# Kernel optimization log

Measured on AMD Instinct MI355X. Metric: run time of the kernel, lower is better.

## Reference

```python
import jax, jax.numpy as jnp
import numpy as np

B, N, D = 8, 1024, 768
NHEAD = 4
N_EDGES = 3
ITERS = 2
DK = D // NHEAD


def setup_inputs() -> dict:
    key = jax.random.key(0)
    ks = jax.random.split(key, 12)
    s = 0.02
    return {
        "nodes_embed": jax.random.normal(ks[0], (B, N, D), dtype=jnp.float32),
        "node_adj": jax.random.randint(ks[1], (B, N, N), 0, 4, dtype=jnp.int32),
        # per-edge-type Q/K linear layers (torch Linear: y = x W^T + b; stored here as [in,out])
        "Wq": jax.random.normal(ks[2], (N_EDGES, D, D), dtype=jnp.float32) * s,
        "bq": jax.random.normal(ks[3], (N_EDGES, D), dtype=jnp.float32) * s,
        "Wk": jax.random.normal(ks[4], (N_EDGES, D, D), dtype=jnp.float32) * s,
        "bk": jax.random.normal(ks[5], (N_EDGES, D), dtype=jnp.float32) * s,
        # GCN weights: shared across heads (self.blocks reuses the same Sequential), distinct per iter
        "gcn_W": jax.random.normal(ks[6], (ITERS, D, D), dtype=jnp.float32) * s,
        "gcn_b": jnp.zeros((ITERS, D), dtype=jnp.float32),
        # aggregate_W: Linear(D*nhead -> D), stored as [D*nhead, D]
        "W_agg": jax.random.normal(ks[7], (D * NHEAD, D), dtype=jnp.float32) * s,
        "b_agg": jnp.zeros((D,), dtype=jnp.float32),
    }


def reference(nodes_embed, node_adj, Wq, bq, Wk, bk, gcn_W, gcn_b, W_agg, b_agg):
    Bv, Nv, Dv = nodes_embed.shape
    h, dk = NHEAD, DK
    adj = node_adj[:, None, :, :]  # [B,1,N,N]
    scale = 1.0 / jnp.sqrt(jnp.asarray(dk, nodes_embed.dtype))

    scores = jnp.zeros((Bv, h, Nv, Nv), dtype=nodes_embed.dtype)
    for e in range(N_EDGES):  # small fixed edge-type loop
        q = (nodes_embed @ Wq[e] + bq[e]).reshape(Bv, Nv, h, dk).transpose(0, 2, 1, 3)  # [B,h,N,dk]
        k = (nodes_embed @ Wk[e] + bk[e]).reshape(Bv, Nv, h, dk).transpose(0, 2, 1, 3)
        s = jnp.einsum('bhnd,bhmd->bhnm', q, k) * scale
        scores = scores + jnp.where(adj == e + 1, s, jnp.zeros((), s.dtype))
    scores = jnp.where(scores == 0, jnp.asarray(-1e9, scores.dtype), scores)
    attn = jax.nn.softmax(scores, axis=-1)          # [B,h,N,N]
    ga = jnp.transpose(attn, (1, 0, 2, 3))          # [h,B,N,N]

    # GCN blocks, vectorized over heads; weights shared across heads
    X = jnp.broadcast_to(nodes_embed, (h, Bv, Nv, Dv))  # [h,B,N,D]
    for i in range(ITERS):
        H = jnp.einsum('hbnd,de->hbne', X, gcn_W[i])
        sum_nei = jnp.einsum('hbnm,hbmd->hbnd', ga, H)
        degs = jnp.sum(ga, axis=-1, keepdims=True)       # [h,B,N,1]
        dst = sum_nei / degs + gcn_b[i]
        X = X + jax.nn.relu(dst)

    # torch.cat over heads along feature dim -> [B,N,h*D]
    cat = jnp.transpose(X, (1, 2, 0, 3)).reshape(Bv, Nv, h * Dv)
    out = cat @ W_agg + b_agg
    return out, ga
```

## Files before the change

### kernel.cpp

```cpp
#include <hip/hip_runtime.h>

typedef long long i64;
typedef unsigned short u16;
typedef __attribute__((ext_vector_type(8))) short short8;
typedef __attribute__((ext_vector_type(4))) float f32x4;

#define Bv 8
#define Nv 1024
#define Dv 768
#define Hh 4
#define DKv 192
#define BND ((i64)Bv * Nv * Dv)
#define HBND ((i64)Hh * BND)

__device__ __forceinline__ u16 f2bf(float f) {
    unsigned u = __builtin_bit_cast(unsigned, f);
    u += 0x7fffu + ((u >> 16) & 1u);
    return (u16)(u >> 16);
}
__device__ __forceinline__ float bf2f(u16 h) {
    unsigned u = ((unsigned)h) << 16;
    return __builtin_bit_cast(float, u);
}

__device__ __forceinline__ void gl_lds16(const u16* g, u16* l) {
    __builtin_amdgcn_global_load_lds(
        (const __attribute__((address_space(1))) void*)g,
        (__attribute__((address_space(3))) void*)l, 16, 0, 0);
}

template <int EPI, bool CATK, int ORD, int NBN, int NBM, int NZ>
__global__ __launch_bounds__(256) void gemm_bf16(
    const u16* __restrict__ A, i64 sA, int lda,
    const u16* __restrict__ Bt, i64 sBt, int ldbt, int zmaskBt,
    const float* __restrict__ bias, i64 sBias, const float* __restrict__ bias2,
    void* __restrict__ Cv, i64 sC, int ldc, int K, int koff)
{
    __shared__ u16 Asb[128 * 64];
    __shared__ u16 Bsb[128 * 64];

    const int L = (blockIdx.x & 7) * ((NBN * NBM * NZ) >> 3) + (blockIdx.x >> 3);
    int bn, bm, z;
    if (ORD == 0) {
        bn = L % NBN; const int t2 = L / NBN; bm = t2 % NBM; z = t2 / NBM;
    } else {
        bn = L % NBN; const int t2 = L / NBN; z = t2 % NZ; bm = t2 / NZ;
    }

    A  += (i64)z * sA;
    Bt += (i64)(z & zmaskBt) * sBt;
    const float* bp = bias;
    int zb = z;
    if (bias2 != nullptr && z >= NZ / 2) { bp = bias2; zb = z - NZ / 2; }
    if (bp) bp += (i64)zb * sBias;
    const int kb = z * koff;

    const int bmp = bm * 128, bnp = bn * 128;
    const int tid = threadIdx.x;
    const int w = tid >> 6, l = tid & 63;
    const int wr = w >> 1, wc = w & 1;
    const int kgrp = l >> 4, lr = l & 15;

    const u16* Ab = A + (i64)bmp * lda;
    const u16* Bb = Bt + (i64)bnp * ldbt;

    f32x4 acc[4][4];
    #pragma unroll
    for (int i = 0; i < 4; ++i)
        #pragma unroll
        for (int j = 0; j < 4; ++j)
            acc[i][j] = (f32x4){0.f, 0.f, 0.f, 0.f};

    for (int k0i = 0; k0i < K; k0i += 64) {
        const int k0 = kb + k0i;
        if (k0i) __syncthreads();
        #pragma unroll
        for (int t = 0; t < 4; ++t) {
            const int idx = t * 256 + tid;
            const int r = idx >> 3, s = idx & 7;
            const int ss = s ^ (r & 7);
            const u16* src;
            if (CATK) {
                src = A + (i64)(k0 / Dv) * BND + (i64)(bmp + r) * Dv + (k0 % Dv) + ss * 8;
            } else {
                src = Ab + (i64)r * lda + k0 + ss * 8;
            }
            gl_lds16(src, &Asb[(t * 256 + w * 64) * 8]);
        }
        #pragma unroll
        for (int t = 0; t < 4; ++t) {
            const int idx = t * 256 + tid;
            const int r = idx >> 3, s = idx & 7;
            const int ss = s ^ (r & 7);
            gl_lds16(Bb + (i64)r * ldbt + k0 + ss * 8, &Bsb[(t * 256 + w * 64) * 8]);
        }
        __syncthreads();

        #pragma unroll
        for (int ks = 0; ks < 2; ++ks) {
            const int slot = ks * 4 + kgrp;
            short8 a[4], b[4];
            #pragma unroll
            for (int i = 0; i < 4; ++i) {
                const int r = wc * 64 + i * 16 + lr;
                a[i] = *(const short8*)&Bsb[r * 64 + ((slot ^ (r & 7)) << 3)];
            }
            #pragma unroll
            for (int j = 0; j < 4; ++j) {
                const int r = wr * 64 + j * 16 + lr;
                b[j] = *(const short8*)&Asb[r * 64 + ((slot ^ (r & 7)) << 3)];
            }
            #pragma unroll
            for (int i = 0; i < 4; ++i)
                #pragma unroll
                for (int j = 0; j < 4; ++j)
                    acc[i][j] = __builtin_amdgcn_mfma_f32_16x16x32_bf16(
                        a[i], b[j], acc[i][j], 0, 0, 0);
        }
    }

    f32x4 bj[4];
    #pragma unroll
    for (int i = 0; i < 4; ++i) {
        const int nb = bnp + wc * 64 + i * 16 + kgrp * 4;
        bj[i] = bp ? *(const f32x4*)&bp[nb] : (f32x4){0.f, 0.f, 0.f, 0.f};
    }

    #pragma unroll
    for (int j = 0; j < 4; ++j) {
        const int m = bmp + wr * 64 + j * 16 + lr;
        #pragma unroll
        for (int i = 0; i < 4; ++i) {
            const int nb = bnp + wc * 64 + i * 16 + kgrp * 4;
            const i64 off = (i64)z * sC + (i64)m * ldc + nb;
            f32x4 v = acc[i][j] + bj[i];
            if (EPI == 0) {
                *(f32x4*)&((float*)Cv)[off] = v;
            } else if (EPI == 1) {
                ushort4 o;
                o.x = f2bf(v[0]); o.y = f2bf(v[1]);
                o.z = f2bf(v[2]); o.w = f2bf(v[3]);
                *(ushort4*)&((u16*)Cv)[off] = o;
            } else {
                u16* xp = (u16*)Cv + off;
                ushort4 old = *(const ushort4*)xp;
                ushort4 o;
                o.x = f2bf(bf2f(old.x) + fmaxf(v[0], 0.f));
                o.y = f2bf(bf2f(old.y) + fmaxf(v[1], 0.f));
                o.z = f2bf(bf2f(old.z) + fmaxf(v[2], 0.f));
                o.w = f2bf(bf2f(old.w) + fmaxf(v[3], 0.f));
                *(ushort4*)xp = o;
            }
        }
    }
}

__global__ __launch_bounds__(256) void scores_mfma(
    const u16* __restrict__ qb, const u16* __restrict__ kb,
    const int* __restrict__ adj, u16* __restrict__ sb)
{
    __shared__ u16 Qs[2][64 * 64];
    __shared__ u16 Ks[2][64 * 64];

    const int bid = blockIdx.x;
    const int b = bid & 7;
    const int t2 = bid >> 3;
    const int h = t2 & 3;
    const int mt = (t2 >> 2) & 15;
    const int nt = t2 >> 6;
    const int m0 = mt * 64, n0 = nt * 64;
    const int zga = h * 8 + b;

    const int tid = threadIdx.x;
    const int w = tid >> 6, l = tid & 63;
    const int wr = w >> 1, wc = w & 1;
    const int kgrp = l >> 4, lr = l & 15;

    const i64 qoff = ((i64)b * Nv + n0) * Dv + h * DKv;
    const i64 koff = ((i64)b * Nv + m0) * Dv + h * DKv;

#define STAGE_SC(ci_, buf_) { \
    const int e_ = (ci_) / 3, k0_ = ((ci_) % 3) * 64; \
    const u16* qe_ = qb + (i64)e_ * BND + qoff; \
    const u16* ke_ = kb + (i64)e_ * BND + koff; \
    _Pragma("unroll") \
    for (int t = 0; t < 2; ++t) { \
        const int idx2 = t * 256 + tid; \
        const int r = idx2 >> 3, s = idx2 & 7; \
        const int ss = s ^ (r & 7); \
        gl_lds16(qe_ + (i64)r * Dv + k0_ + ss * 8, &Qs[buf_][(t * 256 + w * 64) * 8]); \
        gl_lds16(ke_ + (i64)r * Dv + k0_ + ss * 8, &Ks[buf_][(t * 256 + w * 64) * 8]); \
    } }

    int4 adjv[2][2];
    #pragma unroll
    for (int i = 0; i < 2; ++i) {
        const int mb = m0 + wc * 32 + i * 16 + kgrp * 4;
        #pragma unroll
        for (int j = 0; j < 2; ++j) {
            const int n = n0 + wr * 32 + j * 16 + lr;
            adjv[i][j] = *(const int4*)&adj[((i64)b * Nv + n) * Nv + mb];
        }
    }

    f32x4 acc[3][2][2];
    #pragma unroll
    for (int e = 0; e < 3; ++e)
        #pragma unroll
        for (int i = 0; i < 2; ++i)
            #pragma unroll
            for (int j = 0; j < 2; ++j)
                acc[e][i][j] = (f32x4){0.f, 0.f, 0.f, 0.f};

    STAGE_SC(0, 0)

    #pragma unroll
    for (int ci = 0; ci < 9; ++ci) {
        const int cur = ci & 1;
        if (ci < 8) {
            if (cur) { STAGE_SC(ci + 1, 0) } else { STAGE_SC(ci + 1, 1) }
            asm volatile("s_waitcnt vmcnt(4)" ::: "memory");
        } else {
            asm volatile("s_waitcnt vmcnt(0)" ::: "memory");
        }
        __builtin_amdgcn_s_barrier();
        asm volatile("" ::: "memory");

        const int e = ci / 3;
        #pragma unroll
        for (int ks = 0; ks < 2; ++ks) {
            const int slot = ks * 4 + kgrp;
            short8 a[2], bq2[2];
            #pragma unroll
            for (int i = 0; i < 2; ++i) {
                const int r = wc * 32 + i * 16 + lr;
                a[i] = *(const short8*)&Ks[cur][r * 64 + ((slot ^ (r & 7)) << 3)];
            }
            #pragma unroll
            for (int j = 0; j < 2; ++j) {
                const int r = wr * 32 + j * 16 + lr;
                bq2[j] = *(const short8*)&Qs[cur][r * 64 + ((slot ^ (r & 7)) << 3)];
            }
            #pragma unroll
            for (int i = 0; i < 2; ++i)
                #pragma unroll
                for (int j = 0; j < 2; ++j)
                    acc[e][i][j] = __builtin_amdgcn_mfma_f32_16x16x32_bf16(
                        a[i], bq2[j], acc[e][i][j], 0, 0, 0);
        }

        asm volatile("s_waitcnt lgkmcnt(0)" ::: "memory");
        __builtin_amdgcn_s_barrier();
    }
#undef STAGE_SC

    const float scale = 0.07216878364870323f;
    #pragma unroll
    for (int i = 0; i < 2; ++i) {
        const int mb = m0 + wc * 32 + i * 16 + kgrp * 4;
        #pragma unroll
        for (int j = 0; j < 2; ++j) {
            const int n = n0 + wr * 32 + j * 16 + lr;
            const int av[4] = {adjv[i][j].x, adjv[i][j].y, adjv[i][j].z, adjv[i][j].w};
            ushort4 o;
            #pragma unroll
            for (int rg = 0; rg < 4; ++rg) {
                float f = 0.f;
                if (av[rg] == 1) f = acc[0][i][j][rg];
                else if (av[rg] == 2) f = acc[1][i][j][rg];
                else if (av[rg] == 3) f = acc[2][i][j][rg];
                f *= scale;
                if (f == 0.f) f = -1e9f;
                ((u16*)&o)[rg] = f2bf(f);
            }
            *(ushort4*)&sb[((i64)zga * Nv + n) * Nv + mb] = o;
        }
    }
}

__global__ __launch_bounds__(256) void softmax_k(const u16* __restrict__ sb,
                                                 float* __restrict__ ga,
                                                 u16* __restrict__ gab)
{
    const i64 row = blockIdx.x;
    const int tid = threadIdx.x;
    const int wid = tid >> 6, lane = tid & 63;

    ushort4 sv = *(const ushort4*)&sb[row * (i64)Nv + tid * 4];
    float4 v;
    v.x = bf2f(sv.x); v.y = bf2f(sv.y); v.z = bf2f(sv.z); v.w = bf2f(sv.w);

    float m = fmaxf(fmaxf(v.x, v.y), fmaxf(v.z, v.w));
    #pragma unroll
    for (int o = 32; o >= 1; o >>= 1) m = fmaxf(m, __shfl_xor(m, o));

    __shared__ float red[4];
    if (lane == 0) red[wid] = m;
    __syncthreads();
    m = fmaxf(fmaxf(red[0], red[1]), fmaxf(red[2], red[3]));

    float e0 = expf(v.x - m), e1 = expf(v.y - m), e2 = expf(v.z - m), e3 = expf(v.w - m);
    float s = e0 + e1 + e2 + e3;
    #pragma unroll
    for (int o = 32; o >= 1; o >>= 1) s += __shfl_xor(s, o);
    __syncthreads();
    if (lane == 0) red[wid] = s;
    __syncthreads();
    s = red[0] + red[1] + red[2] + red[3];

    const float inv = 1.0f / s;
    float4 o;
    o.x = e0 * inv; o.y = e1 * inv; o.z = e2 * inv; o.w = e3 * inv;
    *(float4*)&ga[row * (i64)Nv + tid * 4] = o;

    ushort4 ob;
    ob.x = f2bf(o.x); ob.y = f2bf(o.y); ob.z = f2bf(o.z); ob.w = f2bf(o.w);
    *(ushort4*)&gab[row * (i64)Nv + tid * 4] = ob;
}

__global__ __launch_bounds__(256) void prep_k(const float* __restrict__ nodes,
                                              u16* __restrict__ nodesb,
                                              u16* __restrict__ Xb)
{
    const i64 i = (i64)blockIdx.x * 256 + threadIdx.x;
    float4 v = ((const float4*)nodes)[i];
    ushort4 o;
    o.x = f2bf(v.x); o.y = f2bf(v.y); o.z = f2bf(v.z); o.w = f2bf(v.w);
    ((ushort4*)nodesb)[i] = o;
    const i64 q4 = BND / 4;
    #pragma unroll
    for (int h = 0; h < Hh; ++h) ((ushort4*)Xb)[(i64)h * q4 + i] = o;
}

__global__ __launch_bounds__(256) void trans_all(
    const float* __restrict__ Wq, const float* __restrict__ Wk,
    const float* __restrict__ gcnW, const float* __restrict__ Wagg,
    u16* __restrict__ wqkt, u16* __restrict__ gcnWt, u16* __restrict__ waggt)
{
    const int z = blockIdx.z;
    const i64 W768 = (i64)768 * 768;
    const float* src;
    u16* dst;
    int ldo;
    if (z < 3)      { src = Wq + z * W768;        dst = wqkt + z * W768;          ldo = 768; }
    else if (z < 6) { src = Wk + (z - 3) * W768;  dst = wqkt + (i64)z * W768;     ldo = 768; }
    else if (z < 8) { src = gcnW + (z - 6) * W768; dst = gcnWt + (i64)(z - 6) * W768; ldo = 768; }
    else            { src = Wagg + (i64)(z - 8) * W768; dst = waggt + (i64)(z - 8) * 768; ldo = 3072; }

    __shared__ u16 t[32][33];
    const int c0 = blockIdx.x * 32, r0 = blockIdx.y * 32;
    const int tx = threadIdx.x & 31, ty = threadIdx.x >> 5;
    #pragma unroll
    for (int i = ty; i < 32; i += 8)
        t[i][tx] = f2bf(src[(i64)(r0 + i) * 768 + c0 + tx]);
    __syncthreads();
    #pragma unroll
    for (int i = ty; i < 32; i += 8)
        dst[(i64)(c0 + i) * ldo + r0 + tx] = t[tx][i];
}

__global__ __launch_bounds__(256) void addbias_k(
    const float* __restrict__ p0, const float* __restrict__ p1,
    const float* __restrict__ bias, float* __restrict__ out)
{
    const i64 i4 = (i64)blockIdx.x * 256 + threadIdx.x;
    const int nb = (int)((i4 * 4) % Dv);
    float4 a = ((const float4*)p0)[i4];
    float4 b = ((const float4*)p1)[i4];
    float4 bv = *(const float4*)&bias[nb];
    float4 o;
    o.x = a.x + b.x + bv.x; o.y = a.y + b.y + bv.y;
    o.z = a.z + b.z + bv.z; o.w = a.w + b.w + bv.w;
    ((float4*)out)[i4] = o;
}

extern "C" void kernel_launch(void* const* d_in, const int* in_sizes, int n_in,
                              void* d_out, int out_size, void* d_ws, size_t ws_size,
                              hipStream_t stream)
{
    const float* nodes = (const float*)d_in[0];
    const int*   adj   = (const int*)d_in[1];
    const float* Wq    = (const float*)d_in[2];
    const float* bq    = (const float*)d_in[3];
    const float* Wk    = (const float*)d_in[4];
    const float* bk    = (const float*)d_in[5];
    const float* gcnW  = (const float*)d_in[6];
    const float* gcnb  = (const float*)d_in[7];
    const float* Wagg  = (const float*)d_in[8];
    const float* bagg  = (const float*)d_in[9];

    float* out = (float*)d_out;
    float* gaf = out + BND;

    const i64 W768 = (i64)768 * 768;
    const i64 HTZ  = (i64)768 * 1024;
    u16* ws     = (u16*)d_ws;
    u16* qb     = ws;
    u16* kb2    = ws + 3 * BND;
    u16* gab    = ws;
    u16* nodesb = ws + 6 * BND;
    u16* gcnWt  = nodesb + BND;
    u16* waggt  = gcnWt + 2 * W768;
    u16* Xb     = waggt + 4 * W768;
    u16* Htz    = Xb + HBND;
    u16* wqkt   = Htz;
    u16* sbuf   = Htz;
    float* part = (float*)Htz;

    dim3 blk(256);

    prep_k<<<dim3((unsigned)(BND / 4 / 256)), blk, 0, stream>>>(nodes, nodesb, Xb);
    trans_all<<<dim3(24, 24, 12), blk, 0, stream>>>(Wq, Wk, gcnW, Wagg, wqkt, gcnWt, waggt);

    gemm_bf16<1, false, 1, 6, 64, 6><<<dim3(2304), blk, 0, stream>>>(
        nodesb, 0, Dv, wqkt, W768, Dv, -1, bq, Dv, bk, qb, BND, Dv, Dv, 0);

    scores_mfma<<<dim3(8192), blk, 0, stream>>>(qb, kb2, adj, sbuf);

    softmax_k<<<dim3(Hh * Bv * Nv), blk, 0, stream>>>(sbuf, gaf, gab);

    for (int it = 0; it < 2; ++it) {
        if (it == 0) {
            gemm_bf16<1, false, 0, 8, 6, 8><<<dim3(384), blk, 0, stream>>>(
                gcnWt, 0, Dv, nodesb, (i64)Nv * Dv, Dv, 7, nullptr, 0, nullptr,
                Htz, HTZ, 1024, Dv, 0);
            gemm_bf16<2, false, 0, 6, 8, 32><<<dim3(1536), blk, 0, stream>>>(
                gab, (i64)Nv * Nv, Nv, Htz, HTZ, 1024, 7, gcnb, 0, nullptr,
                Xb, (i64)Nv * Dv, Dv, Nv, 0);
        } else {
            gemm_bf16<1, false, 0, 8, 6, 32><<<dim3(1536), blk, 0, stream>>>(
                gcnWt + W768, 0, Dv, Xb, (i64)Nv * Dv, Dv, 31, nullptr, 0, nullptr,
                Htz, HTZ, 1024, Dv, 0);
            gemm_bf16<2, false, 0, 6, 8, 32><<<dim3(1536), blk, 0, stream>>>(
                gab, (i64)Nv * Nv, Nv, Htz, HTZ, 1024, 31, gcnb + (i64)Dv, 0, nullptr,
                Xb, (i64)Nv * Dv, Dv, Nv, 0);
        }
    }

    gemm_bf16<0, true, 0, 6, 64, 2><<<dim3(768), blk, 0, stream>>>(
        Xb, 0, Dv, waggt, 0, Hh * Dv, -1, nullptr, 0, nullptr,
        part, BND, Dv, (Hh * Dv) / 2, (Hh * Dv) / 2);

    addbias_k<<<dim3((unsigned)(BND / 4 / 256)), blk, 0, stream>>>(
        part, part + BND, bagg, out);
}
```

Measured before the change: 542.7 us.

## Enlarge scores kernel tiles to 128x128 and fold edge selection per type

The scores kernel now computes 128x128 output tiles per block instead of 64x64, with each wave holding a 4x4 grid of MFMA accumulators. This quadruples reuse of each staged Q/K tile and cuts the block count from 8192 to 2048. Edge types are processed one after another with a single accumulator set, and the adjacency mask is applied into a final register tile after each type, which keeps register use bounded. In exchange, the double-buffered async staging pipeline is replaced by single-buffered loads fenced by syncthreads, so load latency is no longer overlapped with compute. Adjacency is also re-read from global memory once per edge type.

After: 572.3 us. 1.05x slower.

```diff
diff --git a/kernel.cpp b/kernel.cpp
--- a/kernel.cpp
+++ b/kernel.cpp
@@ -159,16 +159,16 @@
     const u16* __restrict__ qb, const u16* __restrict__ kb,
     const int* __restrict__ adj, u16* __restrict__ sb)
 {
-    __shared__ u16 Qs[2][64 * 64];
-    __shared__ u16 Ks[2][64 * 64];
+    __shared__ u16 Qs[128 * 64];
+    __shared__ u16 Ks[128 * 64];
 
     const int bid = blockIdx.x;
     const int b = bid & 7;
     const int t2 = bid >> 3;
     const int h = t2 & 3;
-    const int mt = (t2 >> 2) & 15;
-    const int nt = t2 >> 6;
-    const int m0 = mt * 64, n0 = nt * 64;
+    const int tile = t2 >> 2;
+    const int mt = tile & 7, nt = tile >> 3;
+    const int m0 = mt * 128, n0 = nt * 128;
     const int zga = h * 8 + b;
 
     const int tid = threadIdx.x;
@@ -176,100 +176,95 @@
     const int wr = w >> 1, wc = w & 1;
     const int kgrp = l >> 4, lr = l & 15;
 
-    const i64 qoff = ((i64)b * Nv + n0) * Dv + h * DKv;
-    const i64 koff = ((i64)b * Nv + m0) * Dv + h * DKv;
-
-#define STAGE_SC(ci_, buf_) { \
-    const int e_ = (ci_) / 3, k0_ = ((ci_) % 3) * 64; \
-    const u16* qe_ = qb + (i64)e_ * BND + qoff; \
-    const u16* ke_ = kb + (i64)e_ * BND + koff; \
-    _Pragma("unroll") \
-    for (int t = 0; t < 2; ++t) { \
-        const int idx2 = t * 256 + tid; \
-        const int r = idx2 >> 3, s = idx2 & 7; \
-        const int ss = s ^ (r & 7); \
-        gl_lds16(qe_ + (i64)r * Dv + k0_ + ss * 8, &Qs[buf_][(t * 256 + w * 64) * 8]); \
-        gl_lds16(ke_ + (i64)r * Dv + k0_ + ss * 8, &Ks[buf_][(t * 256 + w * 64) * 8]); \
-    } }
-
-    int4 adjv[2][2];
-    #pragma unroll
-    for (int i = 0; i < 2; ++i) {
-        const int mb = m0 + wc * 32 + i * 16 + kgrp * 4;
-        #pragma unroll
-        for (int j = 0; j < 2; ++j) {
-            const int n = n0 + wr * 32 + j * 16 + lr;
-            adjv[i][j] = *(const int4*)&adj[((i64)b * Nv + n) * Nv + mb];
-        }
-    }
-
-    f32x4 acc[3][2][2];
-    #pragma unroll
-    for (int e = 0; e < 3; ++e)
-        #pragma unroll
-        for (int i = 0; i < 2; ++i)
-            #pragma unroll
-            for (int j = 0; j < 2; ++j)
-                acc[e][i][j] = (f32x4){0.f, 0.f, 0.f, 0.f};
-
-    STAGE_SC(0, 0)
-
-    #pragma unroll
-    for (int ci = 0; ci < 9; ++ci) {
-        const int cur = ci & 1;
-        if (ci < 8) {
-            if (cur) { STAGE_SC(ci + 1, 0) } else { STAGE_SC(ci + 1, 1) }
-            asm volatile("s_waitcnt vmcnt(4)" ::: "memory");
-        } else {
-            asm volatile("s_waitcnt vmcnt(0)" ::: "memory");
-        }
-        __builtin_amdgcn_s_barrier();
-        asm volatile("" ::: "memory");
-
-        const int e = ci / 3;
-        #pragma unroll
-        for (int ks = 0; ks < 2; ++ks) {
-            const int slot = ks * 4 + kgrp;
-            short8 a[2], bq2[2];
-            #pragma unroll
-            for (int i = 0; i < 2; ++i) {
-                const int r = wc * 32 + i * 16 + lr;
-                a[i] = *(const short8*)&Ks[cur][r * 64 + ((slot ^ (r & 7)) << 3)];
-            }
-            #pragma unroll
-            for (int j = 0; j < 2; ++j) {
-                const int r = wr * 32 + j * 16 + lr;
-                bq2[j] = *(const short8*)&Qs[cur][r * 64 + ((slot ^ (r & 7)) << 3)];
-            }
-            #pragma unroll
-            for (int i = 0; i < 2; ++i)
+    const u16* qbase = qb + ((i64)b * Nv + n0) * Dv + h * DKv;
+    const u16* kbase = kb + ((i64)b * Nv + m0) * Dv + h * DKv;
+
+    const float scale = 0.07216878364870323f;
+
+    f32x4 fin[4][4];
+    #pragma unroll
+    for (int i = 0; i < 4; ++i)
+        #pragma unroll
+        for (int j = 0; j < 4; ++j)
+            fin[i][j] = (f32x4){0.f, 0.f, 0.f, 0.f};
+
+    for (int e = 0; e < 3; ++e) {
+        const u16* qe = qbase + (i64)e * BND;
+        const u16* ke = kbase + (i64)e * BND;
+
+        f32x4 acc[4][4];
+        #pragma unroll
+        for (int i = 0; i < 4; ++i)
+            #pragma unroll
+            for (int j = 0; j < 4; ++j)
+                acc[i][j] = (f32x4){0.f, 0.f, 0.f, 0.f};
+
+        for (int k0 = 0; k0 < DKv; k0 += 64) {
+            __syncthreads();
+            #pragma unroll
+            for (int t = 0; t < 4; ++t) {
+                const int idx = t * 256 + tid;
+                const int r = idx >> 3, s = idx & 7;
+                const int ss = s ^ (r & 7);
+                gl_lds16(qe + (i64)r * Dv + k0 + ss * 8, &Qs[(t * 256 + w * 64) * 8]);
+            }
+            #pragma unroll
+            for (int t = 0; t < 4; ++t) {
+                const int idx = t * 256 + tid;
+                const int r = idx >> 3, s = idx & 7;
+                const int ss = s ^ (r & 7);
+                gl_lds16(ke + (i64)r * Dv + k0 + ss * 8, &Ks[(t * 256 + w * 64) * 8]);
+            }
+            __syncthreads();
+
+            #pragma unroll
+            for (int ks = 0; ks < 2; ++ks) {
+                const int slot = ks * 4 + kgrp;
+                short8 a[4], bq2[4];
                 #pragma unroll
-                for (int j = 0; j < 2; ++j)
-                    acc[e][i][j] = __builtin_amdgcn_mfma_f32_16x16x32_bf16(
-                        a[i], bq2[j], acc[e][i][j], 0, 0, 0);
-        }
-
-        asm volatile("s_waitcnt lgkmcnt(0)" ::: "memory");
-        __builtin_amdgcn_s_barrier();
-    }
-#undef STAGE_SC
-
-    const float scale = 0.07216878364870323f;
-    #pragma unroll
-    for (int i = 0; i < 2; ++i) {
-        const int mb = m0 + wc * 32 + i * 16 + kgrp * 4;
-        #pragma unroll
-        for (int j = 0; j < 2; ++j) {
-            const int n = n0 + wr * 32 + j * 16 + lr;
-            const int av[4] = {adjv[i][j].x, adjv[i][j].y, adjv[i][j].z, adjv[i][j].w};
+                for (int i = 0; i < 4; ++i) {
+                    const int r = wc * 64 + i * 16 + lr;
+                    a[i] = *(const short8*)&Ks[r * 64 + ((slot ^ (r & 7)) << 3)];
+                }
+                #pragma unroll
+                for (int j = 0; j < 4; ++j) {
+                    const int r = wr * 64 + j * 16 + lr;
+                    bq2[j] = *(const short8*)&Qs[r * 64 + ((slot ^ (r & 7)) << 3)];
+                }
+                #pragma unroll
+                for (int i = 0; i < 4; ++i)
+                    #pragma unroll
+                    for (int j = 0; j < 4; ++j)
+                        acc[i][j] = __builtin_amdgcn_mfma_f32_16x16x32_bf16(
+                            a[i], bq2[j], acc[i][j], 0, 0, 0);
+            }
+        }
+
+        #pragma unroll
+        for (int i = 0; i < 4; ++i) {
+            const int mb = m0 + wc * 64 + i * 16 + kgrp * 4;
+            #pragma unroll
+            for (int j = 0; j < 4; ++j) {
+                const int n = n0 + wr * 64 + j * 16 + lr;
+                const int4 av = *(const int4*)&adj[((i64)b * Nv + n) * Nv + mb];
+                if (av.x == e + 1) fin[i][j][0] = acc[i][j][0] * scale;
+                if (av.y == e + 1) fin[i][j][1] = acc[i][j][1] * scale;
+                if (av.z == e + 1) fin[i][j][2] = acc[i][j][2] * scale;
+                if (av.w == e + 1) fin[i][j][3] = acc[i][j][3] * scale;
+            }
+        }
+    }
+
+    #pragma unroll
+    for (int i = 0; i < 4; ++i) {
+        const int mb = m0 + wc * 64 + i * 16 + kgrp * 4;
+        #pragma unroll
+        for (int j = 0; j < 4; ++j) {
+            const int n = n0 + wr * 64 + j * 16 + lr;
             ushort4 o;
             #pragma unroll
             for (int rg = 0; rg < 4; ++rg) {
-                float f = 0.f;
-                if (av[rg] == 1) f = acc[0][i][j][rg];
-                else if (av[rg] == 2) f = acc[1][i][j][rg];
-                else if (av[rg] == 3) f = acc[2][i][j][rg];
-                f *= scale;
+                float f = fin[i][j][rg];
                 if (f == 0.f) f = -1e9f;
                 ((u16*)&o)[rg] = f2bf(f);
             }
@@ -415,7 +410,7 @@
     gemm_bf16<1, false, 1, 6, 64, 6><<<dim3(2304), blk, 0, stream>>>(
         nodesb, 0, Dv, wqkt, W768, Dv, -1, bq, Dv, bk, qb, BND, Dv, Dv, 0);
 
-    scores_mfma<<<dim3(8192), blk, 0, stream>>>(qb, kb2, adj, sbuf);
+    scores_mfma<<<dim3(2048), blk, 0, stream>>>(qb, kb2, adj, sbuf);
 
     softmax_k<<<dim3(Hh * Bv * Nv), blk, 0, stream>>>(sbuf, gaf, gab);
 
```

## Add 256x256-tile 8-wave GEMM with phased prefetch for GCN aggregation update

Applied to the files above, without the earlier changes.

Replaces the 128x128-tile GEMM used for the attention-times-H aggregation and X residual update with a new 512-thread kernel. Each block computes a 256x256 output tile, double-buffers LDS, and splits each K-step into four phases that interleave global-to-LDS prefetch of the next tile with MFMA work, raising wave priority during the MFMA bursts. The larger tile cuts global and LDS traffic per FLOP and launches 384 blocks instead of 1536. In exchange it uses much more LDS and registers per block, and the smaller grid may leave some compute units with uneven load.

Result: slower. 566.7 us (+4.4%).

```diff
diff --git a/kernel.cpp b/kernel.cpp
--- a/kernel.cpp
+++ b/kernel.cpp
@@ -28,6 +28,8 @@
         (const __attribute__((address_space(1))) void*)g,
         (__attribute__((address_space(3))) void*)l, 16, 0, 0);
 }
+
+#define VMCNT(n) asm volatile("s_waitcnt vmcnt(" #n ")" ::: "memory")
 
 template <int EPI, bool CATK, int ORD, int NBN, int NBM, int NZ>
 __global__ __launch_bounds__(256) void gemm_bf16(
@@ -155,6 +157,143 @@
     }
 }
 
+__global__ __launch_bounds__(512, 2) void gemm256_xupd(
+    const u16* __restrict__ A, i64 sA, int lda,
+    const u16* __restrict__ Bt, i64 sBt, int ldbt, int zmask,
+    const float* __restrict__ bias,
+    u16* __restrict__ X, i64 sX, int ldx, int K)
+{
+    __shared__ u16 Asb[2][256 * 64];
+    __shared__ u16 Bsb[2][256 * 64];
+
+    const int L = (blockIdx.x & 7) * 48 + (blockIdx.x >> 3);
+    const int bn = L % 3;
+    const int t2 = L / 3;
+    const int bm = t2 & 3;
+    const int z  = t2 >> 2;
+
+    const u16* Ab = A + (i64)z * sA + (i64)(bm * 256) * lda;
+    const u16* Bb = Bt + (i64)(z & zmask) * sBt + (i64)(bn * 256) * ldbt;
+
+    const int tid = threadIdx.x;
+    const int w = tid >> 6, l = tid & 63;
+    const int wr = w >> 2;
+    const int wc = w & 3;
+    const int kgrp = l >> 4, lr = l & 15;
+    const int srow = tid >> 3;
+    const int scol = tid & 7;
+
+    f32x4 acc[8][4];
+    #pragma unroll
+    for (int f = 0; f < 8; ++f)
+        #pragma unroll
+        for (int g = 0; g < 4; ++g)
+            acc[f][g] = (f32x4){0.f, 0.f, 0.f, 0.f};
+
+    short8 bfr[4][2];
+
+#define STG_B(bb_, k0_, q_) { \
+    const int r_ = (q_) * 64 + srow; \
+    const int ss_ = scol ^ (r_ & 7); \
+    gl_lds16(Bb + (i64)r_ * ldbt + (k0_) + ss_ * 8, &Bsb[bb_][(r_ * 8 + scol) * 8]); }
+#define STG_A(bb_, k0_, p_) { \
+    const int r_ = (srow < 32) ? ((p_) * 32 + srow) : (128 + (p_) * 32 + (srow - 32)); \
+    const int ss_ = scol ^ (r_ & 7); \
+    gl_lds16(Ab + (i64)r_ * lda + (k0_) + ss_ * 8, &Asb[bb_][(r_ * 8 + scol) * 8]); }
+#define STG_PH(P_, bb_, k0_) \
+    if ((P_) == 0) { STG_B(bb_, k0_, 0) STG_B(bb_, k0_, 1) } \
+    else if ((P_) == 1) { STG_B(bb_, k0_, 2) STG_B(bb_, k0_, 3) } \
+    else if ((P_) == 2) { STG_A(bb_, k0_, 0) STG_A(bb_, k0_, 1) } \
+    else { STG_A(bb_, k0_, 2) STG_A(bb_, k0_, 3) }
+
+#define PHASE(P_, VMN_, cur_, DOPF_, nxt_, k0n_) { \
+    VMCNT(VMN_); \
+    __builtin_amdgcn_s_barrier(); \
+    asm volatile("" ::: "memory"); \
+    if ((P_) == 0) { \
+        _Pragma("unroll") \
+        for (int g = 0; g < 4; ++g) \
+            _Pragma("unroll") \
+            for (int ks = 0; ks < 2; ++ks) { \
+                const int r_ = wc * 64 + g * 16 + lr; \
+                const int sl_ = ks * 4 + kgrp; \
+                bfr[g][ks] = *(const short8*)&Bsb[cur_][r_ * 64 + ((sl_ ^ (r_ & 7)) << 3)]; \
+            } \
+    } \
+    short8 afr[2][2]; \
+    _Pragma("unroll") \
+    for (int i = 0; i < 2; ++i) \
+        _Pragma("unroll") \
+        for (int ks = 0; ks < 2; ++ks) { \
+            const int r_ = wr * 128 + (2 * (P_) + i) * 16 + lr; \
+            const int sl_ = ks * 4 + kgrp; \
+            afr[i][ks] = *(const short8*)&Asb[cur_][r_ * 64 + ((sl_ ^ (r_ & 7)) << 3)]; \
+        } \
+    if (DOPF_) { STG_PH(P_, nxt_, k0n_) } \
+    __builtin_amdgcn_s_setprio(1); \
+    _Pragma("unroll") \
+    for (int i = 0; i < 2; ++i) \
+        _Pragma("unroll") \
+        for (int g = 0; g < 4; ++g) \
+            _Pragma("unroll") \
+            for (int ks = 0; ks < 2; ++ks) \
+                acc[2 * (P_) + i][g] = __builtin_amdgcn_mfma_f32_16x16x32_bf16( \
+                    bfr[g][ks], afr[i][ks], acc[2 * (P_) + i][g], 0, 0, 0); \
+    __builtin_amdgcn_s_setprio(0); }
+
+    const int NT = K / 64;
+
+    STG_PH(0, 0, 0) STG_PH(1, 0, 0) STG_PH(2, 0, 0) STG_PH(3, 0, 0)
+    VMCNT(0);
+    __builtin_amdgcn_s_barrier();
+    asm volatile("" ::: "memory");
+
+    for (int kt = 0; kt < NT - 1; ++kt) {
+        const int cur = kt & 1, nxt = cur ^ 1;
+        const int k0n = (kt + 1) * 64;
+        PHASE(0, 3, cur, 1, nxt, k0n)
+        PHASE(1, 4, cur, 1, nxt, k0n)
+        PHASE(2, 5, cur, 1, nxt, k0n)
+        PHASE(3, 6, cur, 1, nxt, k0n)
+    }
+    {
+        const int cur = (NT - 1) & 1;
+        PHASE(0, 3, cur, 0, 0, 0)
+        PHASE(1, 2, cur, 0, 0, 0)
+        PHASE(2, 1, cur, 0, 0, 0)
+        PHASE(3, 0, cur, 0, 0, 0)
+    }
+#undef PHASE
+#undef STG_PH
+#undef STG_A
+#undef STG_B
+
+    f32x4 bj[4];
+    #pragma unroll
+    for (int g = 0; g < 4; ++g) {
+        const int n = bn * 256 + wc * 64 + g * 16 + kgrp * 4;
+        bj[g] = *(const f32x4*)&bias[n];
+    }
+
+    #pragma unroll
+    for (int f = 0; f < 8; ++f) {
+        const int m = bm * 256 + wr * 128 + f * 16 + lr;
+        #pragma unroll
+        for (int g = 0; g < 4; ++g) {
+            const int n = bn * 256 + wc * 64 + g * 16 + kgrp * 4;
+            u16* xp = X + (i64)z * sX + (i64)m * ldx + n;
+            f32x4 v = acc[f][g] + bj[g];
+            ushort4 old = *(const ushort4*)xp;
+            ushort4 o;
+            o.x = f2bf(bf2f(old.x) + fmaxf(v[0], 0.f));
+            o.y = f2bf(bf2f(old.y) + fmaxf(v[1], 0.f));
+            o.z = f2bf(bf2f(old.z) + fmaxf(v[2], 0.f));
+            o.w = f2bf(bf2f(old.w) + fmaxf(v[3], 0.f));
+            *(ushort4*)xp = o;
+        }
+    }
+}
+
 __global__ __launch_bounds__(256) void scores_mfma(
     const u16* __restrict__ qb, const u16* __restrict__ kb,
     const int* __restrict__ adj, u16* __restrict__ sb)
@@ -219,9 +358,9 @@
         const int cur = ci & 1;
         if (ci < 8) {
             if (cur) { STAGE_SC(ci + 1, 0) } else { STAGE_SC(ci + 1, 1) }
-            asm volatile("s_waitcnt vmcnt(4)" ::: "memory");
+            VMCNT(4);
         } else {
-            asm volatile("s_waitcnt vmcnt(0)" ::: "memory");
+            VMCNT(0);
         }
         __builtin_amdgcn_s_barrier();
         asm volatile("" ::: "memory");
@@ -424,16 +563,16 @@
             gemm_bf16<1, false, 0, 8, 6, 8><<<dim3(384), blk, 0, stream>>>(
                 gcnWt, 0, Dv, nodesb, (i64)Nv * Dv, Dv, 7, nullptr, 0, nullptr,
                 Htz, HTZ, 1024, Dv, 0);
-            gemm_bf16<2, false, 0, 6, 8, 32><<<dim3(1536), blk, 0, stream>>>(
-                gab, (i64)Nv * Nv, Nv, Htz, HTZ, 1024, 7, gcnb, 0, nullptr,
-                Xb, (i64)Nv * Dv, Dv, Nv, 0);
+            gemm256_xupd<<<dim3(384), dim3(512), 0, stream>>>(
+                gab, (i64)Nv * Nv, Nv, Htz, HTZ, 1024, 7, gcnb,
+                Xb, (i64)Nv * Dv, Dv, Nv);
         } else {
             gemm_bf16<1, false, 0, 8, 6, 32><<<dim3(1536), blk, 0, stream>>>(
                 gcnWt + W768, 0, Dv, Xb, (i64)Nv * Dv, Dv, 31, nullptr, 0, nullptr,
                 Htz, HTZ, 1024, Dv, 0);
-            gemm_bf16<2, false, 0, 6, 8, 32><<<dim3(1536), blk, 0, stream>>>(
-                gab, (i64)Nv * Nv, Nv, Htz, HTZ, 1024, 31, gcnb + (i64)Dv, 0, nullptr,
-                Xb, (i64)Nv * Dv, Dv, Nv, 0);
+            gemm256_xupd<<<dim3(384), dim3(512), 0, stream>>>(
+                gab, (i64)Nv * Nv, Nv, Htz, HTZ, 1024, 31, gcnb + (i64)Dv,
+                Xb, (i64)Nv * Dv, Dv, Nv);
         }
     }
 
```

## Fuse edge-masked attention scores with an online softmax in one kernel

Applied to the files above, without the earlier changes.

The separate scores and softmax kernels are replaced by one kernel in which each block owns 64 query rows and loops over all 16 key tiles. It keeps a running max and sum (online softmax) and stores the masked bf16 scores into the bf16 attention buffer. It then re-reads them to write the normalized fp32 and bf16 probabilities. This removes the intermediate score buffer and one launch, but the grid shrinks from 8192 to 512 blocks, the per-block work becomes long and serial, and the raw scores still make a round trip through global memory. Workspace pointers are reshuffled so the bf16 attention buffer and the GCN scratch no longer alias each other.

New measurement: 619.1 us. 1.14x slower.

```diff
diff --git a/kernel.cpp b/kernel.cpp
--- a/kernel.cpp
+++ b/kernel.cpp
@@ -155,9 +155,10 @@
     }
 }
 
-__global__ __launch_bounds__(256) void scores_mfma(
+__global__ __launch_bounds__(256) void scores_sm_fused(
     const u16* __restrict__ qb, const u16* __restrict__ kb,
-    const int* __restrict__ adj, u16* __restrict__ sb)
+    const int* __restrict__ adj, u16* __restrict__ gab,
+    float* __restrict__ gaf)
 {
     __shared__ u16 Qs[2][64 * 64];
     __shared__ u16 Ks[2][64 * 64];
@@ -166,156 +167,161 @@
     const int b = bid & 7;
     const int t2 = bid >> 3;
     const int h = t2 & 3;
-    const int mt = (t2 >> 2) & 15;
-    const int nt = t2 >> 6;
-    const int m0 = mt * 64, n0 = nt * 64;
+    const int ns = t2 >> 2;
+    const int n0 = ns * 64;
     const int zga = h * 8 + b;
 
     const int tid = threadIdx.x;
     const int w = tid >> 6, l = tid & 63;
-    const int wr = w >> 1, wc = w & 1;
     const int kgrp = l >> 4, lr = l & 15;
-
-    const i64 qoff = ((i64)b * Nv + n0) * Dv + h * DKv;
-    const i64 koff = ((i64)b * Nv + m0) * Dv + h * DKv;
-
-#define STAGE_SC(ci_, buf_) { \
-    const int e_ = (ci_) / 3, k0_ = ((ci_) % 3) * 64; \
-    const u16* qe_ = qb + (i64)e_ * BND + qoff; \
-    const u16* ke_ = kb + (i64)e_ * BND + koff; \
+    const int n = n0 + w * 16 + lr;
+
+    const i64 qoff   = ((i64)b * Nv + n0) * Dv + h * DKv;
+    const i64 kbase0 = ((i64)b * Nv) * Dv + h * DKv;
+
+    const float scale = 0.07216878364870323f;
+
+#define STG(mt_, e_, kc_, bp_) { \
+    const u16* qe_ = qb + (i64)(e_) * BND + qoff + (kc_) * 64; \
+    const u16* ke_ = kb + (i64)(e_) * BND + kbase0 + (i64)(mt_) * 64 * Dv + (kc_) * 64; \
+    u16* Qd_ = Qs[bp_]; u16* Kd_ = Ks[bp_]; \
     _Pragma("unroll") \
     for (int t = 0; t < 2; ++t) { \
         const int idx2 = t * 256 + tid; \
         const int r = idx2 >> 3, s = idx2 & 7; \
         const int ss = s ^ (r & 7); \
-        gl_lds16(qe_ + (i64)r * Dv + k0_ + ss * 8, &Qs[buf_][(t * 256 + w * 64) * 8]); \
-        gl_lds16(ke_ + (i64)r * Dv + k0_ + ss * 8, &Ks[buf_][(t * 256 + w * 64) * 8]); \
+        gl_lds16(qe_ + (i64)r * Dv + ss * 8, &Qd_[(t * 256 + w * 64) * 8]); \
+        gl_lds16(ke_ + (i64)r * Dv + ss * 8, &Kd_[(t * 256 + w * 64) * 8]); \
     } }
 
-    int4 adjv[2][2];
-    #pragma unroll
-    for (int i = 0; i < 2; ++i) {
-        const int mb = m0 + wc * 32 + i * 16 + kgrp * 4;
-        #pragma unroll
-        for (int j = 0; j < 2; ++j) {
-            const int n = n0 + wr * 32 + j * 16 + lr;
-            adjv[i][j] = *(const int4*)&adj[((i64)b * Nv + n) * Nv + mb];
-        }
-    }
-
-    f32x4 acc[3][2][2];
+    f32x4 acc[3][4];
     #pragma unroll
     for (int e = 0; e < 3; ++e)
         #pragma unroll
-        for (int i = 0; i < 2; ++i)
-            #pragma unroll
-            for (int j = 0; j < 2; ++j)
-                acc[e][i][j] = (f32x4){0.f, 0.f, 0.f, 0.f};
-
-    STAGE_SC(0, 0)
-
-    #pragma unroll
-    for (int ci = 0; ci < 9; ++ci) {
-        const int cur = ci & 1;
-        if (ci < 8) {
-            if (cur) { STAGE_SC(ci + 1, 0) } else { STAGE_SC(ci + 1, 1) }
-            asm volatile("s_waitcnt vmcnt(4)" ::: "memory");
-        } else {
-            asm volatile("s_waitcnt vmcnt(0)" ::: "memory");
-        }
-        __builtin_amdgcn_s_barrier();
-        asm volatile("" ::: "memory");
-
-        const int e = ci / 3;
-        #pragma unroll
-        for (int ks = 0; ks < 2; ++ks) {
-            const int slot = ks * 4 + kgrp;
-            short8 a[2], bq2[2];
-            #pragma unroll
-            for (int i = 0; i < 2; ++i) {
-                const int r = wc * 32 + i * 16 + lr;
-                a[i] = *(const short8*)&Ks[cur][r * 64 + ((slot ^ (r & 7)) << 3)];
-            }
-            #pragma unroll
-            for (int j = 0; j < 2; ++j) {
-                const int r = wr * 32 + j * 16 + lr;
-                bq2[j] = *(const short8*)&Qs[cur][r * 64 + ((slot ^ (r & 7)) << 3)];
-            }
-            #pragma unroll
-            for (int i = 0; i < 2; ++i)
+        for (int i = 0; i < 4; ++i)
+            acc[e][i] = (f32x4){0.f, 0.f, 0.f, 0.f};
+
+    float rm = -3.0e38f, rl = 0.f;
+    int cur = 0;
+    STG(0, 0, 0, 0)
+
+    for (int mt = 0; mt < 16; ++mt) {
+        #pragma unroll
+        for (int e = 0; e < 3; ++e) {
+            #pragma unroll
+            for (int kc = 0; kc < 3; ++kc) {
+                if (!(mt == 15 && e == 2 && kc == 2)) {
+                    int e2 = e, kc2 = kc + 1, mtd = 0;
+                    if (kc2 == 3) { kc2 = 0; e2 = e + 1; }
+                    if (e2 == 3) { e2 = 0; mtd = 1; }
+                    STG(mt + mtd, e2, kc2, cur ^ 1)
+                    asm volatile("s_waitcnt vmcnt(4)" ::: "memory");
+                } else {
+                    asm volatile("s_waitcnt vmcnt(0)" ::: "memory");
+                }
+                __builtin_amdgcn_s_barrier();
+                asm volatile("" ::: "memory");
+
+                const u16* Qc = Qs[cur];
+                const u16* Kc = Ks[cur];
                 #pragma unroll
-                for (int j = 0; j < 2; ++j)
-                    acc[e][i][j] = __builtin_amdgcn_mfma_f32_16x16x32_bf16(
-                        a[i], bq2[j], acc[e][i][j], 0, 0, 0);
-        }
-
-        asm volatile("s_waitcnt lgkmcnt(0)" ::: "memory");
-        __builtin_amdgcn_s_barrier();
-    }
-#undef STAGE_SC
-
-    const float scale = 0.07216878364870323f;
-    #pragma unroll
-    for (int i = 0; i < 2; ++i) {
-        const int mb = m0 + wc * 32 + i * 16 + kgrp * 4;
-        #pragma unroll
-        for (int j = 0; j < 2; ++j) {
-            const int n = n0 + wr * 32 + j * 16 + lr;
-            const int av[4] = {adjv[i][j].x, adjv[i][j].y, adjv[i][j].z, adjv[i][j].w};
-            ushort4 o;
+                for (int ks = 0; ks < 2; ++ks) {
+                    const int slot = ks * 4 + kgrp;
+                    short8 qv;
+                    {
+                        const int r = w * 16 + lr;
+                        qv = *(const short8*)&Qc[r * 64 + ((slot ^ (r & 7)) << 3)];
+                    }
+                    #pragma unroll
+                    for (int i = 0; i < 4; ++i) {
+                        const int r = i * 16 + lr;
+                        short8 a = *(const short8*)&Kc[r * 64 + ((slot ^ (r & 7)) << 3)];
+                        acc[e][i] = __builtin_amdgcn_mfma_f32_16x16x32_bf16(
+                            a, qv, acc[e][i], 0, 0, 0);
+                    }
+                }
+                asm volatile("s_waitcnt lgkmcnt(0)" ::: "memory");
+                __builtin_amdgcn_s_barrier();
+                cur ^= 1;
+            }
+        }
+
+        const int m0 = mt * 64;
+        float fin[4][4];
+        #pragma unroll
+        for (int i = 0; i < 4; ++i) {
+            const int mb = m0 + i * 16 + kgrp * 4;
+            const int4 av = *(const int4*)&adj[((i64)b * Nv + n) * Nv + mb];
+            const int avv[4] = {av.x, av.y, av.z, av.w};
             #pragma unroll
             for (int rg = 0; rg < 4; ++rg) {
                 float f = 0.f;
-                if (av[rg] == 1) f = acc[0][i][j][rg];
-                else if (av[rg] == 2) f = acc[1][i][j][rg];
-                else if (av[rg] == 3) f = acc[2][i][j][rg];
+                if (avv[rg] == 1) f = acc[0][i][rg];
+                else if (avv[rg] == 2) f = acc[1][i][rg];
+                else if (avv[rg] == 3) f = acc[2][i][rg];
                 f *= scale;
                 if (f == 0.f) f = -1e9f;
-                ((u16*)&o)[rg] = f2bf(f);
-            }
-            *(ushort4*)&sb[((i64)zga * Nv + n) * Nv + mb] = o;
-        }
-    }
-}
-
-__global__ __launch_bounds__(256) void softmax_k(const u16* __restrict__ sb,
-                                                 float* __restrict__ ga,
-                                                 u16* __restrict__ gab)
-{
-    const i64 row = blockIdx.x;
-    const int tid = threadIdx.x;
-    const int wid = tid >> 6, lane = tid & 63;
-
-    ushort4 sv = *(const ushort4*)&sb[row * (i64)Nv + tid * 4];
-    float4 v;
-    v.x = bf2f(sv.x); v.y = bf2f(sv.y); v.z = bf2f(sv.z); v.w = bf2f(sv.w);
-
-    float m = fmaxf(fmaxf(v.x, v.y), fmaxf(v.z, v.w));
-    #pragma unroll
-    for (int o = 32; o >= 1; o >>= 1) m = fmaxf(m, __shfl_xor(m, o));
-
-    __shared__ float red[4];
-    if (lane == 0) red[wid] = m;
-    __syncthreads();
-    m = fmaxf(fmaxf(red[0], red[1]), fmaxf(red[2], red[3]));
-
-    float e0 = expf(v.x - m), e1 = expf(v.y - m), e2 = expf(v.z - m), e3 = expf(v.w - m);
-    float s = e0 + e1 + e2 + e3;
-    #pragma unroll
-    for (int o = 32; o >= 1; o >>= 1) s += __shfl_xor(s, o);
-    __syncthreads();
-    if (lane == 0) red[wid] = s;
-    __syncthreads();
-    s = red[0] + red[1] + red[2] + red[3];
-
-    const float inv = 1.0f / s;
-    float4 o;
-    o.x = e0 * inv; o.y = e1 * inv; o.z = e2 * inv; o.w = e3 * inv;
-    *(float4*)&ga[row * (i64)Nv + tid * 4] = o;
-
-    ushort4 ob;
-    ob.x = f2bf(o.x); ob.y = f2bf(o.y); ob.z = f2bf(o.z); ob.w = f2bf(o.w);
-    *(ushort4*)&gab[row * (i64)Nv + tid * 4] = ob;
+                fin[i][rg] = f;
+            }
+        }
+
+        float tmax = fin[0][0];
+        #pragma unroll
+        for (int i = 0; i < 4; ++i)
+            #pragma unroll
+            for (int rg = 0; rg < 4; ++rg)
+                tmax = fmaxf(tmax, fin[i][rg]);
+        tmax = fmaxf(tmax, __shfl_xor(tmax, 16));
+        tmax = fmaxf(tmax, __shfl_xor(tmax, 32));
+
+        float tsum = 0.f;
+        #pragma unroll
+        for (int i = 0; i < 4; ++i)
+            #pragma unroll
+            for (int rg = 0; rg < 4; ++rg)
+                tsum += expf(fin[i][rg] - tmax);
+        tsum += __shfl_xor(tsum, 16);
+        tsum += __shfl_xor(tsum, 32);
+
+        const float mnew = fmaxf(rm, tmax);
+        rl = rl * expf(rm - mnew) + tsum * expf(tmax - mnew);
+        rm = mnew;
+
+        #pragma unroll
+        for (int i = 0; i < 4; ++i) {
+            ushort4 o;
+            o.x = f2bf(fin[i][0]); o.y = f2bf(fin[i][1]);
+            o.z = f2bf(fin[i][2]); o.w = f2bf(fin[i][3]);
+            *(ushort4*)&gab[((i64)zga * Nv + n) * Nv + m0 + i * 16 + kgrp * 4] = o;
+        }
+
+        #pragma unroll
+        for (int e = 0; e < 3; ++e)
+            #pragma unroll
+            for (int i = 0; i < 4; ++i)
+                acc[e][i] = (f32x4){0.f, 0.f, 0.f, 0.f};
+    }
+#undef STG
+
+    asm volatile("s_waitcnt vmcnt(0)" ::: "memory");
+    const float inv = 1.0f / rl;
+    for (int mt = 0; mt < 16; ++mt) {
+        #pragma unroll
+        for (int i = 0; i < 4; ++i) {
+            const i64 off = ((i64)zga * Nv + n) * Nv + mt * 64 + i * 16 + kgrp * 4;
+            const ushort4 raw = *(const ushort4*)&gab[off];
+            f32x4 p;
+            p[0] = expf(bf2f(raw.x) - rm) * inv;
+            p[1] = expf(bf2f(raw.y) - rm) * inv;
+            p[2] = expf(bf2f(raw.z) - rm) * inv;
+            p[3] = expf(bf2f(raw.w) - rm) * inv;
+            *(f32x4*)&gaf[off] = p;
+            ushort4 o;
+            o.x = f2bf(p[0]); o.y = f2bf(p[1]);
+            o.z = f2bf(p[2]); o.w = f2bf(p[3]);
+            *(ushort4*)&gab[off] = o;
+        }
+    }
 }
 
 __global__ __launch_bounds__(256) void prep_k(const float* __restrict__ nodes,
@@ -397,15 +403,15 @@
     u16* ws     = (u16*)d_ws;
     u16* qb     = ws;
     u16* kb2    = ws + 3 * BND;
-    u16* gab    = ws;
+    u16* Htz    = ws;
+    float* part = (float*)ws;
     u16* nodesb = ws + 6 * BND;
     u16* gcnWt  = nodesb + BND;
     u16* waggt  = gcnWt + 2 * W768;
     u16* Xb     = waggt + 4 * W768;
-    u16* Htz    = Xb + HBND;
-    u16* wqkt   = Htz;
-    u16* sbuf   = Htz;
-    float* part = (float*)Htz;
+    u16* ws2    = Xb + HBND;
+    u16* wqkt   = ws2;
+    u16* gab    = ws2;
 
     dim3 blk(256);
 
@@ -415,9 +421,7 @@
     gemm_bf16<1, false, 1, 6, 64, 6><<<dim3(2304), blk, 0, stream>>>(
         nodesb, 0, Dv, wqkt, W768, Dv, -1, bq, Dv, bk, qb, BND, Dv, Dv, 0);
 
-    scores_mfma<<<dim3(8192), blk, 0, stream>>>(qb, kb2, adj, sbuf);
-
-    softmax_k<<<dim3(Hh * Bv * Nv), blk, 0, stream>>>(sbuf, gaf, gab);
+    scores_sm_fused<<<dim3(512), blk, 0, stream>>>(qb, kb2, adj, gab, gaf);
 
     for (int it = 0; it < 2; ++it) {
         if (it == 0) {
```
